# Optimization experiments

Measured on AMD Instinct MI355X. Metric: run time of the kernel, lower is better.

Reference implementation:

```python
import jax, jax.numpy as jnp
import numpy as np

N_WIRES = 16
N_LAYERS = 4
BATCH = 256
DIM = 2 ** N_WIRES


def _rot_u(theta):
    # theta: (3,) = (rx, ry, rz) angles. Combined single-qubit unitary
    # U = RZ(rz) @ RY(ry) @ RX(rx), matching the gate application order
    # RX -> RY -> RZ in the circuit.
    a, b, c = theta[0] * 0.5, theta[1] * 0.5, theta[2] * 0.5
    cx = jnp.cos(a).astype(jnp.complex64)
    sx = jnp.sin(a).astype(jnp.complex64)
    cy = jnp.cos(b).astype(jnp.complex64)
    sy = jnp.sin(b).astype(jnp.complex64)
    RX = jnp.stack([jnp.stack([cx, -1j * sx]), jnp.stack([-1j * sx, cx])])
    RY = jnp.stack([jnp.stack([cy, -sy]), jnp.stack([sy, cy])])
    ez = jnp.exp(-1j * c.astype(jnp.complex64))
    RZ = jnp.stack([jnp.stack([ez, 0 * ez]), jnp.stack([0 * ez, jnp.conj(ez)])])
    return RZ @ (RY @ RX)


def _apply_1q(psi, U, q):
    # psi: [B] + [2]*n ; apply 2x2 unitary U on qubit axis q
    psi = jnp.moveaxis(psi, 1 + q, -1)
    psi = psi @ U.T  # new[i] = sum_j U[i,j] psi[j]
    return jnp.moveaxis(psi, -1, 1 + q)


def _apply_cnot(psi, c, t):
    # control qubit c, target qubit t
    psi = jnp.moveaxis(psi, (1 + c, 1 + t), (-2, -1))  # [..., 2(c), 2(t)]
    psi = jnp.stack([psi[..., 0, :], psi[..., 1, ::-1]], axis=-2)
    return jnp.moveaxis(psi, (-2, -1), (1 + c, 1 + t))


def _forward(state_batch, params, w_head, b_head):
    B = state_batch.shape[0]
    psi = state_batch.astype(jnp.complex64).reshape((B,) + (2,) * N_WIRES)
    # Precompute all fused RZ*RY*RX unitaries: [L, n, 2, 2]
    Us = jax.vmap(jax.vmap(_rot_u))(params)
    for layer in range(N_LAYERS):
        for q in range(N_WIRES):
            psi = _apply_1q(psi, Us[layer, q], q)
        for q in range(N_WIRES - 1):
            psi = _apply_cnot(psi, q, q + 1)
    psi = psi.reshape(B, DIM)
    probs = psi.real ** 2 + psi.imag ** 2  # [B, DIM], float32
    # PauliZ expectation per wire; wire 0 is the most significant bit
    idx = jnp.arange(DIM)[:, None]
    bits = (idx >> (N_WIRES - 1 - jnp.arange(N_WIRES))) & 1  # [DIM, n]
    signs = (1 - 2 * bits).astype(jnp.float32)
    features = probs @ signs  # [B, n]
    out = features @ w_head.T + b_head  # [B, 1]
    return out[:, 0]


def setup_inputs() -> dict:
    key = jax.random.key(0)
    k1, k2, k3, k4 = jax.random.split(key, 4)
    state = jax.random.normal(k1, (BATCH, DIM), jnp.float32)
    state = state / jnp.linalg.norm(state, axis=-1, keepdims=True)
    params = jax.random.normal(k2, (N_LAYERS, N_WIRES, 3), jnp.float32)
    w_head = jax.random.normal(k3, (1, N_WIRES), jnp.float32) / np.float32(np.sqrt(N_WIRES))
    b_head = jax.random.normal(k4, (1,), jnp.float32) * 0.01
    return {"state_batch": state, "params": params, "w_head": w_head, "b_head": b_head}


def reference(state_batch, params, w_head, b_head):
    return _forward(state_batch, params, w_head, b_head)
```

## Files before the change

### kernel.cpp

```cpp
#include <hip/hip_runtime.h>

typedef float v2f __attribute__((ext_vector_type(2)));

#define NT 512
#define NR 16

__device__ __forceinline__ int swz(int l) { return l ^ ((l >> 5) & 31); }

__device__ __forceinline__ void rot2(v2f& x, v2f& y, v2f aa, v2f an, v2f bb, v2f bn) {
  v2f xs = __builtin_shufflevector(x, x, 1, 0);
  v2f ys = __builtin_shufflevector(y, y, 1, 0);
  v2f n0 = aa * x + an * xs + bb * y + bn * ys;
  v2f n1 = aa * y - an * ys + bn * xs - bb * x;
  x = n0;
  y = n1;
}

#define ROT(T, G)                                                              \
  do {                                                                         \
    const float4 u = Utab[G];                                                  \
    const v2f aa = {u.x, u.x}, an = {-u.y, u.y};                               \
    const v2f bb = {u.z, u.z}, bn = {-u.w, u.w};                               \
    _Pragma("unroll") for (int v = 0; v < NR; ++v) if (!((v >> (T)) & 1))      \
        rot2(s[v], s[v | (1 << (T))], aa, an, bb, bn);                         \
  } while (0)

#define CNOTW(C, T)                                                            \
  do {                                                                         \
    _Pragma("unroll") for (int v = 0; v < NR; ++v)                             \
        if (((v >> (C)) & 1) && !((v >> (T)) & 1)) {                           \
      v2f tmp = s[v];                                                          \
      s[v] = s[v | (1 << (T))];                                                \
      s[v | (1 << (T))] = tmp;                                                 \
    }                                                                          \
  } while (0)

#define MAP_A1(t, v) (((v) << 9) | (t))
#define MAP_A2(t, v) ((((t) >> 6) << 10) | ((v) << 6) | ((t) & 63))
#define MAP_A3(t, v) ((((t) >> 3) << 7) | ((v) << 3) | ((t) & 7))
#define MAP_A4(t, v) (((t) << 4) | (v))
#define MAP_B2(t, v) ((((t) >> 2) << 6) | ((v) << 2) | ((t) & 3))
#define MAP_B3(t, v) ((((t) >> 1) << 5) | ((v) << 1) | ((t) & 1))

#define REMAP_W(MW)                                                            \
  _Pragma("unroll") for (int r = 0; r < NR; ++r) lds2[swz(MW(tid, r))] = s[r]
#define REMAP_R(MR)                                                            \
  _Pragma("unroll") for (int v = 0; v < NR; ++v) s[v] = lds2[swz(MR(tid, v))]

#define REMAP_L(MW, MR)  do { REMAP_W(MW); REMAP_R(MR); } while (0)
#define REMAP_BWB(MW, MR) do { __syncthreads(); REMAP_W(MW); __syncthreads(); REMAP_R(MR); } while (0)
#define REMAP_WB(MW, MR)  do { REMAP_W(MW); __syncthreads(); REMAP_R(MR); } while (0)

__global__ void k_setup(const float* __restrict__ params, float4* __restrict__ Utab) {
  int g = threadIdx.x;
  if (g < 64) {
    float a = params[g * 3 + 0] * 0.5f;
    float b = params[g * 3 + 1] * 0.5f;
    float c = params[g * 3 + 2] * 0.5f;
    float sa, ca, sb, cb, sc, cc;
    sincosf(a, &sa, &ca);
    sincosf(b, &sb, &cb);
    sincosf(c, &sc, &cc);
    float X = cb * ca, Y = sb * sa;
    float Xp = -sb * ca, Yp = -cb * sa;
    Utab[g] = make_float4(cc * X + sc * Y, cc * Y - sc * X,
                          cc * Xp + sc * Yp, cc * Yp - sc * Xp);
  }
}

__global__ __launch_bounds__(NT, 2) void k_passA(const float* __restrict__ in,
                                                 const float4* __restrict__ Utab,
                                                 v2f* __restrict__ st) {
  __shared__ v2f lds2[8192];
  const int tid = threadIdx.x;
  const int g = (blockIdx.x >> 3) & 7;
  const int b = ((blockIdx.x >> 6) << 3) | (blockIdx.x & 7);
  const float* base = in + (size_t)b * 65536;

  v2f s[NR];
#pragma unroll
  for (int v = 0; v < NR; ++v) {
    float re = base[(v << 12) + (tid << 3) + g];
    s[v] = v2f{re, 0.0f};
  }

#pragma unroll
  for (int l = 0; l < 4; ++l) {
    ROT(3, l * 16 + 0); ROT(2, l * 16 + 1); ROT(1, l * 16 + 2); ROT(0, l * 16 + 3);
    CNOTW(3, 2); CNOTW(2, 1); CNOTW(1, 0);
    REMAP_BWB(MAP_A1, MAP_A2);
    ROT(2, l * 16 + 4); ROT(1, l * 16 + 5); ROT(0, l * 16 + 6);
    CNOTW(3, 2); CNOTW(2, 1); CNOTW(1, 0);
    REMAP_L(MAP_A2, MAP_A3);
    ROT(2, l * 16 + 7); ROT(1, l * 16 + 8); ROT(0, l * 16 + 9);
    CNOTW(3, 2); CNOTW(2, 1); CNOTW(1, 0);
    if (l < 3) {
      REMAP_L(MAP_A3, MAP_A4);
      ROT(2, l * 16 + 10);
      if (l <= 1) ROT(1, l * 16 + 11);
      if (l == 0) ROT(0, l * 16 + 12);
      CNOTW(3, 2);
      if (l <= 1) CNOTW(2, 1);
      if (l == 0) CNOTW(1, 0);
      REMAP_WB(MAP_A4, MAP_A1);
    }
  }

  REMAP_W(MAP_A3);
  __syncthreads();
  float4* outp = (float4*)(st + (size_t)(b * 8 + g) * 8192);
#pragma unroll
  for (int k = 0; k < 8; ++k) {
    int o = (k << 10) + (tid << 1);
    v2f a0 = lds2[swz(o)], a1 = lds2[swz(o + 1)];
    outp[(k << 9) + tid] = make_float4(a0[0], a0[1], a1[0], a1[1]);
  }
}

__global__ __launch_bounds__(NT, 2) void k_passB(const v2f* __restrict__ st,
                                                 const float4* __restrict__ Utab,
                                                 float* __restrict__ partials) {
  __shared__ v2f lds2[8192];
  const int tid = threadIdx.x;
  const int b = blockIdx.x >> 3;
  const int h = blockIdx.x & 7;
  const float4* base4 = (const float4*)(st + (size_t)b * 65536);

#pragma unroll
  for (int k = 0; k < 8; ++k) {
    float4 val = base4[(k << 12) + (h << 9) + tid];
    int i = tid << 1;
    lds2[swz(((i) << 3) | k)] = v2f{val.x, val.y};
    lds2[swz(((i + 1) << 3) | k)] = v2f{val.z, val.w};
  }
  v2f s[NR];
  REMAP_R(MAP_A4);

  ROT(2, 13); ROT(1, 14); ROT(0, 15);
  CNOTW(3, 2); CNOTW(2, 1); CNOTW(1, 0);
  ROT(3, 28); ROT(2, 29); ROT(1, 30); ROT(0, 31);
  REMAP_L(MAP_A4, MAP_A3);
  CNOTW(1, 0);
  ROT(1, 43);
  CNOTW(2, 1);
  ROT(2, 58);
  CNOTW(3, 2);
  REMAP_L(MAP_A3, MAP_B2);
  CNOTW(1, 0);
  ROT(1, 44);
  CNOTW(2, 1);
  ROT(2, 59);
  CNOTW(3, 2);
  REMAP_L(MAP_B2, MAP_B3);
  CNOTW(1, 0);
  ROT(1, 45);
  CNOTW(2, 1);
  ROT(2, 60);
  CNOTW(3, 2);
  REMAP_L(MAP_B3, MAP_A4);
  CNOTW(1, 0);
  ROT(1, 46); ROT(0, 47);
  CNOTW(2, 1); CNOTW(1, 0);
  ROT(2, 61); ROT(1, 62); ROT(0, 63);
  CNOTW(3, 2); CNOTW(2, 1); CNOTW(1, 0);

  float P = 0.f, f12 = 0.f, f13 = 0.f, f14 = 0.f, f15 = 0.f;
#pragma unroll
  for (int v = 0; v < NR; ++v) {
    float p = s[v][0] * s[v][0] + s[v][1] * s[v][1];
    P += p;
    f12 += ((v >> 3) & 1) ? -p : p;
    f13 += ((v >> 2) & 1) ? -p : p;
    f14 += ((v >> 1) & 1) ? -p : p;
    f15 += ((v >> 0) & 1) ? -p : p;
  }
  float vals[14];
  vals[0] = P;
#pragma unroll
  for (int q = 3; q <= 11; ++q)
    vals[q - 2] = ((tid >> (11 - q)) & 1) ? -P : P;
  vals[10] = f12; vals[11] = f13; vals[12] = f14; vals[13] = f15;

  const int lane = tid & 63, w = tid >> 6;
#pragma unroll
  for (int q = 0; q < 14; ++q) {
    float x = vals[q];
#pragma unroll
    for (int m = 1; m < 64; m <<= 1) x += __shfl_xor(x, m, 64);
    vals[q] = x;
  }
  __syncthreads();
  float* red = (float*)lds2;
  if (lane == 0) {
#pragma unroll
    for (int q = 0; q < 14; ++q) red[q * 8 + w] = vals[q];
  }
  __syncthreads();
  if (tid < 14) {
    float F = 0.f;
#pragma unroll
    for (int ww = 0; ww < 8; ++ww) F += red[tid * 8 + ww];
    float* pt = partials + (size_t)blockIdx.x * 16;
    if (tid == 0) {
      pt[0] = (h & 4) ? -F : F;
      pt[1] = (h & 2) ? -F : F;
      pt[2] = (h & 1) ? -F : F;
    } else {
      pt[tid + 2] = F;
    }
  }
}

__global__ void k_head(const float* __restrict__ partials, const float* __restrict__ w,
                       const float* __restrict__ bh, float* __restrict__ out) {
  int b = threadIdx.x;
  float acc = bh[0];
  for (int q = 0; q < 16; ++q) {
    float F = 0.f;
    for (int hh = 0; hh < 8; ++hh) F += partials[(size_t)(b * 8 + hh) * 16 + q];
    acc += w[q] * F;
  }
  out[b] = acc;
}

extern "C" void kernel_launch(void* const* d_in, const int* in_sizes, int n_in,
                              void* d_out, int out_size, void* d_ws, size_t ws_size,
                              hipStream_t stream) {
  const float* state  = (const float*)d_in[0];
  const float* params = (const float*)d_in[1];
  const float* w_head = (const float*)d_in[2];
  const float* b_head = (const float*)d_in[3];
  float* out = (float*)d_out;

  char* ws = (char*)d_ws;
  v2f* st = (v2f*)ws;
  float4* Utab = (float4*)(ws + (size_t)134217728);
  float* partials = (float*)(ws + (size_t)134217728 + 1024);

  k_setup<<<1, 64, 0, stream>>>(params, Utab);
  k_passA<<<dim3(2048), dim3(NT), 0, stream>>>(state, Utab, st);
  k_passB<<<dim3(2048), dim3(NT), 0, stream>>>(st, Utab, partials);
  k_head<<<1, 256, 0, stream>>>(partials, w_head, b_head, out);
}
```

Baseline: 209.4 us.

## Split state into 12-qubit tiles with 256-thread blocks and re-schedule gate passes

Pass A now simulates a 12-qubit sub-state per block instead of 13, using 256 threads and half the LDS, and runs twice as many blocks. The gate schedule, remap layouts and the split of gates between pass A and pass B are redone to match, and pass B reads the intermediate state straight into registers instead of staging it through LDS. The goal is higher occupancy from less LDS per block and simpler coalesced global I/O. In exchange, pass B needs more LDS remaps and more partial sums.

```diff
diff --git a/kernel.cpp b/kernel.cpp
--- a/kernel.cpp
+++ b/kernel.cpp
@@ -2,7 +2,7 @@
 
 typedef float v2f __attribute__((ext_vector_type(2)));
 
-#define NT 512
+#define NT 256
 #define NR 16
 
 __device__ __forceinline__ int swz(int l) { return l ^ ((l >> 5) & 31); }
@@ -35,12 +35,13 @@
     }                                                                          \
   } while (0)
 
-#define MAP_A1(t, v) (((v) << 9) | (t))
-#define MAP_A2(t, v) ((((t) >> 6) << 10) | ((v) << 6) | ((t) & 63))
-#define MAP_A3(t, v) ((((t) >> 3) << 7) | ((v) << 3) | ((t) & 7))
-#define MAP_A4(t, v) (((t) << 4) | (v))
-#define MAP_B2(t, v) ((((t) >> 2) << 6) | ((v) << 2) | ((t) & 3))
-#define MAP_B3(t, v) ((((t) >> 1) << 5) | ((v) << 1) | ((t) & 1))
+#define MAP_W1(t, v)  (((v) << 8) | (t))
+#define MAP_W2(t, v)  ((((t) >> 5) << 9) | ((v) << 5) | ((t) & 31))
+#define MAP_W3(t, v)  ((((t) >> 2) << 6) | ((v) << 2) | ((t) & 3))
+#define MAP_W4(t, v)  (((t) << 4) | (v))
+#define MAP_B3(t, v)  ((((t) >> 1) << 5) | ((v) << 1) | ((t) & 1))
+#define MAP_C4(t, v)  ((((t) >> 4) << 8) | ((v) << 4) | ((t) & 15))
+#define MAP_D63(t, v) ((((t) >> 3) << 7) | ((v) << 3) | ((t) & 7))
 
 #define REMAP_W(MW)                                                            \
   _Pragma("unroll") for (int r = 0; r < NR; ++r) lds2[swz(MW(tid, r))] = s[r]
@@ -68,19 +69,21 @@
   }
 }
 
-__global__ __launch_bounds__(NT, 2) void k_passA(const float* __restrict__ in,
+__global__ __launch_bounds__(NT, 4) void k_passA(const float* __restrict__ in,
                                                  const float4* __restrict__ Utab,
                                                  v2f* __restrict__ st) {
-  __shared__ v2f lds2[8192];
+  __shared__ v2f lds2[4096];
   const int tid = threadIdx.x;
-  const int g = (blockIdx.x >> 3) & 7;
-  const int b = ((blockIdx.x >> 6) << 3) | (blockIdx.x & 7);
+  const int xcd = blockIdx.x & 7;
+  const int y = blockIdx.x >> 3;
+  const int g = y & 15;
+  const int b = xcd | ((y >> 4) << 3);
   const float* base = in + (size_t)b * 65536;
 
   v2f s[NR];
 #pragma unroll
   for (int v = 0; v < NR; ++v) {
-    float re = base[(v << 12) + (tid << 3) + g];
+    float re = base[(v << 12) + (tid << 4) + g];
     s[v] = v2f{re, 0.0f};
   }
 
@@ -88,80 +91,80 @@
   for (int l = 0; l < 4; ++l) {
     ROT(3, l * 16 + 0); ROT(2, l * 16 + 1); ROT(1, l * 16 + 2); ROT(0, l * 16 + 3);
     CNOTW(3, 2); CNOTW(2, 1); CNOTW(1, 0);
-    REMAP_BWB(MAP_A1, MAP_A2);
+    REMAP_BWB(MAP_W1, MAP_W2);
     ROT(2, l * 16 + 4); ROT(1, l * 16 + 5); ROT(0, l * 16 + 6);
     CNOTW(3, 2); CNOTW(2, 1); CNOTW(1, 0);
-    REMAP_L(MAP_A2, MAP_A3);
-    ROT(2, l * 16 + 7); ROT(1, l * 16 + 8); ROT(0, l * 16 + 9);
-    CNOTW(3, 2); CNOTW(2, 1); CNOTW(1, 0);
-    if (l < 3) {
-      REMAP_L(MAP_A3, MAP_A4);
-      ROT(2, l * 16 + 10);
-      if (l <= 1) ROT(1, l * 16 + 11);
-      if (l == 0) ROT(0, l * 16 + 12);
-      CNOTW(3, 2);
-      if (l <= 1) CNOTW(2, 1);
-      if (l == 0) CNOTW(1, 0);
-      REMAP_WB(MAP_A4, MAP_A1);
+    REMAP_L(MAP_W2, MAP_W3);
+    ROT(2, l * 16 + 7); ROT(1, l * 16 + 8);
+    if (l <= 2) ROT(0, l * 16 + 9);
+    CNOTW(3, 2); CNOTW(2, 1);
+    if (l <= 2) CNOTW(1, 0);
+    if (l <= 1) {
+      REMAP_L(MAP_W3, MAP_W4);
+      if (l == 0) { ROT(1, 10); ROT(0, 11); CNOTW(2, 1); CNOTW(1, 0); }
+      else        { ROT(1, 16 + 10); CNOTW(2, 1); }
+      REMAP_WB(MAP_W4, MAP_W1);
+    } else if (l == 2) {
+      REMAP_WB(MAP_W3, MAP_W1);
     }
   }
 
-  REMAP_W(MAP_A3);
+  REMAP_W(MAP_W3);
   __syncthreads();
-  float4* outp = (float4*)(st + (size_t)(b * 8 + g) * 8192);
-#pragma unroll
-  for (int k = 0; k < 8; ++k) {
-    int o = (k << 10) + (tid << 1);
-    v2f a0 = lds2[swz(o)], a1 = lds2[swz(o + 1)];
-    outp[(k << 9) + tid] = make_float4(a0[0], a0[1], a1[0], a1[1]);
-  }
-}
-
-__global__ __launch_bounds__(NT, 2) void k_passB(const v2f* __restrict__ st,
+  v2f* outp = st + (size_t)(b * 16 + g) * 4096;
+#pragma unroll
+  for (int k = 0; k < 16; ++k) outp[(k << 8) + tid] = lds2[swz((k << 8) | tid)];
+}
+
+__global__ __launch_bounds__(NT, 4) void k_passB(const v2f* __restrict__ st,
                                                  const float4* __restrict__ Utab,
                                                  float* __restrict__ partials) {
-  __shared__ v2f lds2[8192];
+  __shared__ v2f lds2[4096];
   const int tid = threadIdx.x;
-  const int b = blockIdx.x >> 3;
-  const int h = blockIdx.x & 7;
-  const float4* base4 = (const float4*)(st + (size_t)b * 65536);
-
-#pragma unroll
-  for (int k = 0; k < 8; ++k) {
-    float4 val = base4[(k << 12) + (h << 9) + tid];
-    int i = tid << 1;
-    lds2[swz(((i) << 3) | k)] = v2f{val.x, val.y};
-    lds2[swz(((i + 1) << 3) | k)] = v2f{val.z, val.w};
-  }
+  const int b = blockIdx.x >> 4;
+  const int h = blockIdx.x & 15;
+  const v2f* base = st + (size_t)b * 65536;
+
   v2f s[NR];
-  REMAP_R(MAP_A4);
-
-  ROT(2, 13); ROT(1, 14); ROT(0, 15);
+#pragma unroll
+  for (int v = 0; v < NR; ++v) s[v] = base[(size_t)v * 4096 + (h << 8) + tid];
+
+  ROT(3, 12); ROT(2, 13); ROT(1, 14); ROT(0, 15);
+  REMAP_L(MAP_W4, MAP_B3);
   CNOTW(3, 2); CNOTW(2, 1); CNOTW(1, 0);
-  ROT(3, 28); ROT(2, 29); ROT(1, 30); ROT(0, 31);
-  REMAP_L(MAP_A4, MAP_A3);
-  CNOTW(1, 0);
-  ROT(1, 43);
-  CNOTW(2, 1);
-  ROT(2, 58);
-  CNOTW(3, 2);
-  REMAP_L(MAP_A3, MAP_B2);
-  CNOTW(1, 0);
-  ROT(1, 44);
-  CNOTW(2, 1);
-  ROT(2, 59);
-  CNOTW(3, 2);
-  REMAP_L(MAP_B2, MAP_B3);
-  CNOTW(1, 0);
-  ROT(1, 45);
-  CNOTW(2, 1);
-  ROT(2, 60);
-  CNOTW(3, 2);
-  REMAP_L(MAP_B3, MAP_A4);
-  CNOTW(1, 0);
-  ROT(1, 46); ROT(0, 47);
+  ROT(3, 16 + 11); ROT(2, 16 + 12); ROT(1, 16 + 13);
+  REMAP_L(MAP_B3, MAP_W4);
+  CNOTW(1, 0);
+  ROT(1, 16 + 14); ROT(0, 16 + 15);
+  REMAP_L(MAP_W4, MAP_C4);
+  CNOTW(1, 0);
+  ROT(1, 32 + 10);
+  CNOTW(2, 1);
+  ROT(2, 48 + 9);
+  CNOTW(3, 2);
+  REMAP_L(MAP_C4, MAP_D63);
+  CNOTW(1, 0);
+  ROT(1, 32 + 11);
+  CNOTW(2, 1);
+  ROT(2, 48 + 10);
+  CNOTW(3, 2);
+  REMAP_L(MAP_D63, MAP_W3);
+  CNOTW(1, 0);
+  ROT(1, 32 + 12);
+  CNOTW(2, 1);
+  ROT(2, 48 + 11);
+  CNOTW(3, 2);
+  REMAP_L(MAP_W3, MAP_B3);
+  CNOTW(1, 0);
+  ROT(1, 32 + 13);
+  CNOTW(2, 1);
+  ROT(2, 48 + 12);
+  CNOTW(3, 2);
+  REMAP_L(MAP_B3, MAP_W4);
+  CNOTW(1, 0);
+  ROT(1, 32 + 14); ROT(0, 32 + 15);
   CNOTW(2, 1); CNOTW(1, 0);
-  ROT(2, 61); ROT(1, 62); ROT(0, 63);
+  ROT(2, 48 + 13); ROT(1, 48 + 14); ROT(0, 48 + 15);
   CNOTW(3, 2); CNOTW(2, 1); CNOTW(1, 0);
 
   float P = 0.f, f12 = 0.f, f13 = 0.f, f14 = 0.f, f15 = 0.f;
@@ -174,16 +177,16 @@
     f14 += ((v >> 1) & 1) ? -p : p;
     f15 += ((v >> 0) & 1) ? -p : p;
   }
-  float vals[14];
+  float vals[13];
   vals[0] = P;
 #pragma unroll
-  for (int q = 3; q <= 11; ++q)
-    vals[q - 2] = ((tid >> (11 - q)) & 1) ? -P : P;
-  vals[10] = f12; vals[11] = f13; vals[12] = f14; vals[13] = f15;
+  for (int q = 4; q <= 11; ++q)
+    vals[q - 3] = ((tid >> (11 - q)) & 1) ? -P : P;
+  vals[9] = f12; vals[10] = f13; vals[11] = f14; vals[12] = f15;
 
   const int lane = tid & 63, w = tid >> 6;
 #pragma unroll
-  for (int q = 0; q < 14; ++q) {
+  for (int q = 0; q < 13; ++q) {
     float x = vals[q];
 #pragma unroll
     for (int m = 1; m < 64; m <<= 1) x += __shfl_xor(x, m, 64);
@@ -193,20 +196,21 @@
   float* red = (float*)lds2;
   if (lane == 0) {
 #pragma unroll
-    for (int q = 0; q < 14; ++q) red[q * 8 + w] = vals[q];
+    for (int q = 0; q < 13; ++q) red[q * 4 + w] = vals[q];
   }
   __syncthreads();
-  if (tid < 14) {
+  if (tid < 13) {
     float F = 0.f;
 #pragma unroll
-    for (int ww = 0; ww < 8; ++ww) F += red[tid * 8 + ww];
+    for (int ww = 0; ww < 4; ++ww) F += red[tid * 4 + ww];
     float* pt = partials + (size_t)blockIdx.x * 16;
     if (tid == 0) {
-      pt[0] = (h & 4) ? -F : F;
-      pt[1] = (h & 2) ? -F : F;
-      pt[2] = (h & 1) ? -F : F;
+      pt[0] = (h & 8) ? -F : F;
+      pt[1] = (h & 4) ? -F : F;
+      pt[2] = (h & 2) ? -F : F;
+      pt[3] = (h & 1) ? -F : F;
     } else {
-      pt[tid + 2] = F;
+      pt[tid + 3] = F;
     }
   }
 }
@@ -217,7 +221,7 @@
   float acc = bh[0];
   for (int q = 0; q < 16; ++q) {
     float F = 0.f;
-    for (int hh = 0; hh < 8; ++hh) F += partials[(size_t)(b * 8 + hh) * 16 + q];
+    for (int hh = 0; hh < 16; ++hh) F += partials[(size_t)(b * 16 + hh) * 16 + q];
     acc += w[q] * F;
   }
   out[b] = acc;
@@ -238,7 +242,7 @@
   float* partials = (float*)(ws + (size_t)134217728 + 1024);
 
   k_setup<<<1, 64, 0, stream>>>(params, Utab);
-  k_passA<<<dim3(2048), dim3(NT), 0, stream>>>(state, Utab, st);
-  k_passB<<<dim3(2048), dim3(NT), 0, stream>>>(st, Utab, partials);
+  k_passA<<<dim3(4096), dim3(NT), 0, stream>>>(state, Utab, st);
+  k_passB<<<dim3(4096), dim3(NT), 0, stream>>>(st, Utab, partials);
   k_head<<<1, 256, 0, stream>>>(partials, w_head, b_head, out);
 }
```

Result: slower. 222.1 us (+6.1%).

## Repartition quantum circuit passes: 12-qubit pass A tiles and direct-load pass B

Applied to the files above, without the earlier changes.

Pass A now runs 256-thread blocks, each holding a 4096-amplitude slice (12 qubits), over twice as many blocks. Pass B's 4 prefix-qubit rotations for the last layers move into pass B, and its gate order and LDS remap sequence are rearranged to match. Pass B now loads its intermediate state straight into registers with float4 reads instead of staging it through LDS first. The aim is higher occupancy and less LDS traffic per pass, at the cost of strided 8-byte stores from pass A and a more intricate gate schedule across the split.

```diff
diff --git a/kernel.cpp b/kernel.cpp
--- a/kernel.cpp
+++ b/kernel.cpp
@@ -2,7 +2,8 @@
 
 typedef float v2f __attribute__((ext_vector_type(2)));
 
-#define NT 512
+#define NTA 256
+#define NTB 512
 #define NR 16
 
 __device__ __forceinline__ int swz(int l) { return l ^ ((l >> 5) & 31); }
@@ -16,40 +17,51 @@
   y = n1;
 }
 
-#define ROT(T, G)                                                              \
+#define ROTS(S, T, G)                                                          \
   do {                                                                         \
     const float4 u = Utab[G];                                                  \
     const v2f aa = {u.x, u.x}, an = {-u.y, u.y};                               \
     const v2f bb = {u.z, u.z}, bn = {-u.w, u.w};                               \
     _Pragma("unroll") for (int v = 0; v < NR; ++v) if (!((v >> (T)) & 1))      \
-        rot2(s[v], s[v | (1 << (T))], aa, an, bb, bn);                         \
+        rot2(S[v], S[v | (1 << (T))], aa, an, bb, bn);                         \
   } while (0)
 
-#define CNOTW(C, T)                                                            \
+#define CNOTS(S, C, T)                                                         \
   do {                                                                         \
     _Pragma("unroll") for (int v = 0; v < NR; ++v)                             \
         if (((v >> (C)) & 1) && !((v >> (T)) & 1)) {                           \
-      v2f tmp = s[v];                                                          \
-      s[v] = s[v | (1 << (T))];                                                \
-      s[v | (1 << (T))] = tmp;                                                 \
+      v2f tmp = S[v];                                                          \
+      S[v] = S[v | (1 << (T))];                                                \
+      S[v | (1 << (T))] = tmp;                                                 \
     }                                                                          \
   } while (0)
 
-#define MAP_A1(t, v) (((v) << 9) | (t))
-#define MAP_A2(t, v) ((((t) >> 6) << 10) | ((v) << 6) | ((t) & 63))
-#define MAP_A3(t, v) ((((t) >> 3) << 7) | ((v) << 3) | ((t) & 7))
-#define MAP_A4(t, v) (((t) << 4) | (v))
-#define MAP_B2(t, v) ((((t) >> 2) << 6) | ((v) << 2) | ((t) & 3))
-#define MAP_B3(t, v) ((((t) >> 1) << 5) | ((v) << 1) | ((t) & 1))
-
-#define REMAP_W(MW)                                                            \
-  _Pragma("unroll") for (int r = 0; r < NR; ++r) lds2[swz(MW(tid, r))] = s[r]
-#define REMAP_R(MR)                                                            \
-  _Pragma("unroll") for (int v = 0; v < NR; ++v) s[v] = lds2[swz(MR(tid, v))]
-
-#define REMAP_L(MW, MR)  do { REMAP_W(MW); REMAP_R(MR); } while (0)
-#define REMAP_BWB(MW, MR) do { __syncthreads(); REMAP_W(MW); __syncthreads(); REMAP_R(MR); } while (0)
-#define REMAP_WB(MW, MR)  do { REMAP_W(MW); __syncthreads(); REMAP_R(MR); } while (0)
+#define MAP_W1(t, v)  (((v) << 8) | (t))
+#define MAP_W2(t, v)  ((((t) >> 5) << 9) | ((v) << 5) | ((t) & 31))
+#define MAP_W3(t, v)  ((((t) >> 2) << 6) | ((v) << 2) | ((t) & 3))
+#define MAP_W4(t, v)  (((t) << 4) | (v))
+
+#define M40(t, v) (((t) << 4) | (v))
+#define M41(t, v) ((((t) >> 1) << 5) | ((v) << 1) | ((t) & 1))
+#define M52(t, v) ((((t) >> 2) << 6) | ((v) << 2) | ((t) & 3))
+#define M63(t, v) ((((t) >> 3) << 7) | ((v) << 3) | ((t) & 7))
+#define M74(t, v) ((((t) >> 4) << 8) | ((v) << 4) | ((t) & 15))
+
+#define WM(S, L, M) _Pragma("unroll") for (int r = 0; r < NR; ++r) L[swz(M(tid, r))] = S[r]
+#define RM(S, L, M) _Pragma("unroll") for (int v = 0; v < NR; ++v) S[v] = L[swz(M(tid, v))]
+
+#define GPRE(S) do { ROTS(S,3,12); ROTS(S,2,13); ROTS(S,1,14); ROTS(S,0,15); } while (0)
+#define GQ0(S)  do { CNOTS(S,3,2); CNOTS(S,2,1); CNOTS(S,1,0);                 \
+                     ROTS(S,3,27); ROTS(S,2,28); ROTS(S,1,29); } while (0)
+#define GQ1(S)  do { CNOTS(S,1,0); ROTS(S,1,30); ROTS(S,0,31); } while (0)
+#define GD0(S)  do { CNOTS(S,1,0); ROTS(S,1,42); CNOTS(S,2,1); ROTS(S,2,57); CNOTS(S,3,2); } while (0)
+#define GD1(S)  do { CNOTS(S,1,0); ROTS(S,1,43); CNOTS(S,2,1); ROTS(S,2,58); CNOTS(S,3,2); } while (0)
+#define GD2(S)  do { CNOTS(S,1,0); ROTS(S,1,44); CNOTS(S,2,1); ROTS(S,2,59); CNOTS(S,3,2); } while (0)
+#define GD3(S)  do { CNOTS(S,1,0); ROTS(S,1,45); CNOTS(S,2,1); ROTS(S,2,60); CNOTS(S,3,2); } while (0)
+#define GD4(S)  do { CNOTS(S,1,0); ROTS(S,1,46); ROTS(S,0,47);                 \
+                     CNOTS(S,2,1); CNOTS(S,1,0);                               \
+                     ROTS(S,2,61); ROTS(S,1,62); ROTS(S,0,63);                 \
+                     CNOTS(S,3,2); CNOTS(S,2,1); CNOTS(S,1,0); } while (0)
 
 __global__ void k_setup(const float* __restrict__ params, float4* __restrict__ Utab) {
   int g = threadIdx.x;
@@ -68,101 +80,96 @@
   }
 }
 
-__global__ __launch_bounds__(NT, 2) void k_passA(const float* __restrict__ in,
-                                                 const float4* __restrict__ Utab,
-                                                 v2f* __restrict__ st) {
-  __shared__ v2f lds2[8192];
+__global__ __launch_bounds__(NTA, 4) void k_passA(const float* __restrict__ in,
+                                                  const float4* __restrict__ Utab,
+                                                  v2f* __restrict__ st) {
+  __shared__ v2f lds2[4096];
   const int tid = threadIdx.x;
-  const int g = (blockIdx.x >> 3) & 7;
-  const int b = ((blockIdx.x >> 6) << 3) | (blockIdx.x & 7);
+  const int xcd = blockIdx.x & 7;
+  const int y = blockIdx.x >> 3;
+  const int g = y & 15;
+  const int b = xcd | ((y >> 4) << 3);
   const float* base = in + (size_t)b * 65536;
 
   v2f s[NR];
 #pragma unroll
   for (int v = 0; v < NR; ++v) {
-    float re = base[(v << 12) + (tid << 3) + g];
+    float re = base[(v << 12) + (tid << 4) + g];
     s[v] = v2f{re, 0.0f};
   }
 
 #pragma unroll
   for (int l = 0; l < 4; ++l) {
-    ROT(3, l * 16 + 0); ROT(2, l * 16 + 1); ROT(1, l * 16 + 2); ROT(0, l * 16 + 3);
-    CNOTW(3, 2); CNOTW(2, 1); CNOTW(1, 0);
-    REMAP_BWB(MAP_A1, MAP_A2);
-    ROT(2, l * 16 + 4); ROT(1, l * 16 + 5); ROT(0, l * 16 + 6);
-    CNOTW(3, 2); CNOTW(2, 1); CNOTW(1, 0);
-    REMAP_L(MAP_A2, MAP_A3);
-    ROT(2, l * 16 + 7); ROT(1, l * 16 + 8); ROT(0, l * 16 + 9);
-    CNOTW(3, 2); CNOTW(2, 1); CNOTW(1, 0);
-    if (l < 3) {
-      REMAP_L(MAP_A3, MAP_A4);
-      ROT(2, l * 16 + 10);
-      if (l <= 1) ROT(1, l * 16 + 11);
-      if (l == 0) ROT(0, l * 16 + 12);
-      CNOTW(3, 2);
-      if (l <= 1) CNOTW(2, 1);
-      if (l == 0) CNOTW(1, 0);
-      REMAP_WB(MAP_A4, MAP_A1);
+    ROTS(s, 3, l * 16 + 0); ROTS(s, 2, l * 16 + 1); ROTS(s, 1, l * 16 + 2);
+    ROTS(s, 0, l * 16 + 3);
+    CNOTS(s, 3, 2); CNOTS(s, 2, 1); CNOTS(s, 1, 0);
+    __syncthreads();
+    WM(s, lds2, MAP_W1);
+    __syncthreads();
+    RM(s, lds2, MAP_W2);
+    ROTS(s, 2, l * 16 + 4); ROTS(s, 1, l * 16 + 5); ROTS(s, 0, l * 16 + 6);
+    CNOTS(s, 3, 2); CNOTS(s, 2, 1); CNOTS(s, 1, 0);
+    WM(s, lds2, MAP_W2); RM(s, lds2, MAP_W3);
+    ROTS(s, 2, l * 16 + 7); ROTS(s, 1, l * 16 + 8);
+    if (l <= 2) ROTS(s, 0, l * 16 + 9);
+    CNOTS(s, 3, 2); CNOTS(s, 2, 1);
+    if (l <= 2) CNOTS(s, 1, 0);
+    if (l <= 1) {
+      WM(s, lds2, MAP_W3); RM(s, lds2, MAP_W4);
+      if (l == 0) { ROTS(s, 1, 10); ROTS(s, 0, 11); CNOTS(s, 2, 1); CNOTS(s, 1, 0); }
+      else        { ROTS(s, 1, 26); CNOTS(s, 2, 1); }
+      WM(s, lds2, MAP_W4);
+      __syncthreads();
+      RM(s, lds2, MAP_W1);
+    } else if (l == 2) {
+      WM(s, lds2, MAP_W3);
+      __syncthreads();
+      RM(s, lds2, MAP_W1);
     }
   }
 
-  REMAP_W(MAP_A3);
+  WM(s, lds2, MAP_W3);
   __syncthreads();
-  float4* outp = (float4*)(st + (size_t)(b * 8 + g) * 8192);
-#pragma unroll
-  for (int k = 0; k < 8; ++k) {
-    int o = (k << 10) + (tid << 1);
-    v2f a0 = lds2[swz(o)], a1 = lds2[swz(o + 1)];
-    outp[(k << 9) + tid] = make_float4(a0[0], a0[1], a1[0], a1[1]);
-  }
-}
-
-__global__ __launch_bounds__(NT, 2) void k_passB(const v2f* __restrict__ st,
-                                                 const float4* __restrict__ Utab,
-                                                 float* __restrict__ partials) {
+  v2f* outp = st + (size_t)b * 65536 + ((g >> 1) << 13) + (g & 1);
+#pragma unroll
+  for (int k = 0; k < 16; ++k) {
+    int m = (k << 8) | tid;
+    outp[m << 1] = lds2[swz(m)];
+  }
+}
+
+__global__ __launch_bounds__(NTB, 2) void k_passB(const float4* __restrict__ st4,
+                                                  const float4* __restrict__ Utab,
+                                                  float* __restrict__ partials) {
   __shared__ v2f lds2[8192];
   const int tid = threadIdx.x;
   const int b = blockIdx.x >> 3;
   const int h = blockIdx.x & 7;
-  const float4* base4 = (const float4*)(st + (size_t)b * 65536);
-
-#pragma unroll
-  for (int k = 0; k < 8; ++k) {
-    float4 val = base4[(k << 12) + (h << 9) + tid];
-    int i = tid << 1;
-    lds2[swz(((i) << 3) | k)] = v2f{val.x, val.y};
-    lds2[swz(((i + 1) << 3) | k)] = v2f{val.z, val.w};
-  }
+  const float4* base4 = st4 + (size_t)b * 32768;
+
   v2f s[NR];
-  REMAP_R(MAP_A4);
-
-  ROT(2, 13); ROT(1, 14); ROT(0, 15);
-  CNOTW(3, 2); CNOTW(2, 1); CNOTW(1, 0);
-  ROT(3, 28); ROT(2, 29); ROT(1, 30); ROT(0, 31);
-  REMAP_L(MAP_A4, MAP_A3);
-  CNOTW(1, 0);
-  ROT(1, 43);
-  CNOTW(2, 1);
-  ROT(2, 58);
-  CNOTW(3, 2);
-  REMAP_L(MAP_A3, MAP_B2);
-  CNOTW(1, 0);
-  ROT(1, 44);
-  CNOTW(2, 1);
-  ROT(2, 59);
-  CNOTW(3, 2);
-  REMAP_L(MAP_B2, MAP_B3);
-  CNOTW(1, 0);
-  ROT(1, 45);
-  CNOTW(2, 1);
-  ROT(2, 60);
-  CNOTW(3, 2);
-  REMAP_L(MAP_B3, MAP_A4);
-  CNOTW(1, 0);
-  ROT(1, 46); ROT(0, 47);
-  CNOTW(2, 1); CNOTW(1, 0);
-  ROT(2, 61); ROT(1, 62); ROT(0, 63);
-  CNOTW(3, 2); CNOTW(2, 1); CNOTW(1, 0);
+#pragma unroll
+  for (int g2 = 0; g2 < 8; ++g2) {
+    float4 f = base4[(g2 << 12) + (h << 9) + tid];
+    s[2 * g2]     = v2f{f.x, f.y};
+    s[2 * g2 + 1] = v2f{f.z, f.w};
+  }
+
+  GPRE(s);
+  WM(s, lds2, M40); RM(s, lds2, M41);
+  GQ0(s);
+  WM(s, lds2, M41); RM(s, lds2, M40);
+  GQ1(s);
+  WM(s, lds2, M40); RM(s, lds2, M74);
+  GD0(s);
+  WM(s, lds2, M74); RM(s, lds2, M63);
+  GD1(s);
+  WM(s, lds2, M63); RM(s, lds2, M52);
+  GD2(s);
+  WM(s, lds2, M52); RM(s, lds2, M41);
+  GD3(s);
+  WM(s, lds2, M41); RM(s, lds2, M40);
+  GD4(s);
 
   float P = 0.f, f12 = 0.f, f13 = 0.f, f14 = 0.f, f15 = 0.f;
 #pragma unroll
@@ -238,7 +245,7 @@
   float* partials = (float*)(ws + (size_t)134217728 + 1024);
 
   k_setup<<<1, 64, 0, stream>>>(params, Utab);
-  k_passA<<<dim3(2048), dim3(NT), 0, stream>>>(state, Utab, st);
-  k_passB<<<dim3(2048), dim3(NT), 0, stream>>>(st, Utab, partials);
+  k_passA<<<dim3(4096), dim3(NTA), 0, stream>>>(state, Utab, st);
+  k_passB<<<dim3(2048), dim3(NTB), 0, stream>>>((const float4*)st, Utab, partials);
   k_head<<<1, 256, 0, stream>>>(partials, w_head, b_head, out);
 }
```

New measurement: 216.1 us. 3.2% more time.
